# Kernel tuning notes

Hardware: AMD Instinct MI355X
Metric: run time of the kernel (lower is better)

## Reference

```python
import math
import jax, jax.numpy as jnp
import numpy as np

B, T, HID = 2, 1024, 2048
NH = 2            # num_householder
H = 6             # num_heads
DK = 256          # head_qk_dim
DV = 512          # head_v_dim (expand_v=2)
KEY_DIM = H * DK  # 1536
VAL_DIM = H * DV  # 3072
KCONV = 4
CHUNK = 64        # remat chunk for the scan


def _short_conv(x, w):
    # causal depthwise conv1d + silu. x: [B,T,C], w: [C,K]
    K = w.shape[-1]
    Tt = x.shape[1]
    xp = jnp.pad(x, ((0, 0), (K - 1, 0), (0, 0)))
    y = sum(xp[:, j:j + Tt, :] * w[:, j] for j in range(K))
    return jax.nn.silu(y)


def _interleave(seqs):
    b, t = seqs[0].shape[:2]
    return jnp.stack(seqs, axis=2).reshape(b, t * len(seqs), *seqs[0].shape[2:])


def _l2norm(x):
    return x * jax.lax.rsqrt(jnp.sum(x * x, axis=-1, keepdims=True) + 1e-12)


def _gated_delta_rule(q, k, v, g, beta):
    # q,k: [B,Ti,H,DK], v: [B,Ti,H,DV], g,beta: [B,Ti,H]
    tm = lambda x: jnp.moveaxis(x, 1, 0)  # time-major
    q, k, v, g, beta = map(tm, (q, k, v, g, beta))
    Ti, bsz = q.shape[0], q.shape[1]
    nc = Ti // CHUNK
    rc = lambda x: x.reshape(nc, CHUNK, *x.shape[1:])
    inputs = tuple(map(rc, (q, k, v, g, beta)))

    def step(S, inp):
        qt, kt, vt, gt, bt = inp
        S = S * jnp.exp(gt)[..., None, None]                      # forget gate
        err = vt - jnp.einsum('bhk,bhkv->bhv', kt, S)             # delta-rule error
        u = err * bt[..., None]
        S = S + jnp.einsum('bhk,bhv->bhkv', kt, u)                # rank-1 update
        o_t = jnp.einsum('bhk,bhkv->bhv', qt, S)
        return S, o_t

    @jax.checkpoint
    def chunk_fn(S, ci):
        return jax.lax.scan(step, S, ci)

    S0 = jnp.zeros((bsz, H, DK, DV), q.dtype)
    _, o = jax.lax.scan(chunk_fn, S0, inputs)
    o = o.reshape(Ti, bsz, H, DV)
    return jnp.moveaxis(o, 0, 1)


def setup_inputs() -> dict:
    key = jax.random.key(0)
    ks = jax.random.split(key, 16)
    s = 0.02
    dt = jnp.exp(jax.random.uniform(ks[12], (H,)) * (math.log(0.1) - math.log(0.001)) + math.log(0.001))
    dt = jnp.clip(dt, 1e-4, None)
    return {
        'hidden_states': jax.random.normal(ks[0], (B, T, HID), jnp.float32),
        'q_w': jax.random.normal(ks[1], (HID, KEY_DIM)) * s,
        'k_ws': jax.random.normal(ks[2], (NH, HID, KEY_DIM)) * s,
        'v_ws': jax.random.normal(ks[3], (NH, HID, VAL_DIM)) * s,
        'b_ws': jax.random.normal(ks[4], (NH, HID, H)) * s,
        'a_w': jax.random.normal(ks[5], (HID, H)) * s,
        'g_w': jax.random.normal(ks[6], (HID, VAL_DIM)) * s,
        'o_w': jax.random.normal(ks[7], (VAL_DIM, HID)) * s,
        'q_conv_w': jax.random.normal(ks[8], (KEY_DIM, KCONV)) * 0.3,
        'k_conv_ws': jax.random.normal(ks[9], (NH, KEY_DIM, KCONV)) * 0.3,
        'v_conv_ws': jax.random.normal(ks[10], (NH, VAL_DIM, KCONV)) * 0.3,
        'A_log': jnp.log(jax.random.uniform(ks[11], (H,), minval=0.5, maxval=16.0)),
        'dt_bias': dt + jnp.log(-jnp.expm1(-dt)),
        'o_norm_w': jnp.ones((DV,), jnp.float32),
    }


def reference(hidden_states, q_w, k_ws, v_ws, b_ws, a_w, g_w, o_w,
              q_conv_w, k_conv_ws, v_conv_ws, A_log, dt_bias, o_norm_w):
    x = hidden_states
    ks_list = [_short_conv(x @ k_ws[i], k_conv_ws[i]) for i in range(NH)]
    vs_list = [_short_conv(x @ v_ws[i], v_conv_ws[i]) for i in range(NH)]
    betas = [jax.nn.sigmoid(x @ b_ws[i]) for i in range(NH)]
    q = _short_conv(x @ q_w, q_conv_w)

    # interleave: q only at the last sub-step, g only at the first
    q_i = _interleave([jnp.zeros_like(q)] * (NH - 1) + [q])
    k_i = _interleave(ks_list)
    v_i = _interleave(vs_list)
    beta_i = _interleave(betas)
    g = -jnp.exp(A_log) * jax.nn.softplus(x @ a_w + dt_bias)   # [B,T,H]
    g_i = _interleave([g] + [jnp.zeros_like(g)] * (NH - 1))

    heads = lambda t, d: t.reshape(t.shape[0], t.shape[1], H, d)
    qh = _l2norm(heads(q_i, DK)) * (DK ** -0.5)
    kh = _l2norm(heads(k_i, DK))
    vh = heads(v_i, DV)

    o = _gated_delta_rule(qh, kh, vh, g_i, beta_i)   # [B,T*NH,H,DV]
    o = o[:, NH - 1::NH]                             # [B,T,H,DV]

    gate = heads(x @ g_w, DV)
    rms = o * jax.lax.rsqrt(jnp.mean(o * o, axis=-1, keepdims=True) + 1e-5) * o_norm_w
    o = rms * (gate * jax.nn.sigmoid(gate))          # RMSNorm + swish gate
    return o.reshape(B, T, VAL_DIM) @ o_w
```

## Files before the change

kernel.cpp:

```cpp
#include <hip/hip_runtime.h>


typedef short bf16x8 __attribute__((ext_vector_type(8)));
typedef short bf16x4 __attribute__((ext_vector_type(4)));
typedef float f32x4 __attribute__((ext_vector_type(4)));

__device__ __forceinline__ float bf2f(short s) {
  unsigned u = ((unsigned)(unsigned short)s) << 16;
  float f; __builtin_memcpy(&f, &u, 4); return f;
}
__device__ __forceinline__ short f2bf(float f) {
  unsigned u; __builtin_memcpy(&u, &f, 4);
  u = (u + 0x7FFFu + ((u >> 16) & 1u)) >> 16;
  return (short)u;
}
__device__ __forceinline__ f32x4 MFMA(bf16x8 a, bf16x8 b, f32x4 c) {
  return __builtin_amdgcn_mfma_f32_16x16x32_bf16(a, b, c, 0, 0, 0);
}
__device__ __forceinline__ void gl_lds16(const short* g, short* l) {
  __builtin_amdgcn_global_load_lds(
      (const __attribute__((address_space(1))) unsigned int*)g,
      (__attribute__((address_space(3))) unsigned int*)l, 16, 0, 0);
}

#define PJ_N 13824
#define NTOK 2048

__global__ __launch_bounds__(256) void cvt_bf16(
    const float* __restrict__ src, short* __restrict__ dst, int n)
{
  int i = (blockIdx.x * 256 + threadIdx.x) * 8;
  if (i + 8 <= n) {
    float4 a = *(const float4*)(src + i);
    float4 b = *(const float4*)(src + i + 4);
    short v[8] = {f2bf(a.x), f2bf(a.y), f2bf(a.z), f2bf(a.w),
                  f2bf(b.x), f2bf(b.y), f2bf(b.z), f2bf(b.w)};
    uint4 u; __builtin_memcpy(&u, v, 16);
    *(uint4*)(dst + i) = u;
  }
}

__global__ __launch_bounds__(256) void transpose_w(
    const float* __restrict__ W, short* __restrict__ WT, int K, int N)
{
  __shared__ short tile[64][68];
  const int n0 = blockIdx.x * 64, k0 = blockIdx.y * 64;
  const int lane = threadIdx.x & 63, wv = threadIdx.x >> 6;
  #pragma unroll
  for (int j = 0; j < 16; ++j) {
    int kk = wv * 16 + j;
    tile[kk][lane] = f2bf(W[(size_t)(k0 + kk) * N + n0 + lane]);
  }
  __syncthreads();
  const int nr = threadIdx.x >> 2, seg = (threadIdx.x & 3) * 16;
  short v[16];
  #pragma unroll
  for (int j = 0; j < 16; ++j) v[j] = tile[seg + j][nr];
  uint4 a, b; __builtin_memcpy(&a, v, 16); __builtin_memcpy(&b, v + 8, 16);
  short* dst = WT + (size_t)(n0 + nr) * K + k0 + seg;
  *(uint4*)dst = a;
  *(uint4*)(dst + 8) = b;
}

template<bool F32OUT>
__global__ __launch_bounds__(256) void gemm_bt(
    const short* __restrict__ A, const short* __restrict__ BT,
    void* __restrict__ Cp, int M, int N, int K)
{
  __shared__ short As[128 * 64];
  __shared__ short Bs[128 * 64];
  const int tid = threadIdx.x;
  const int lane = tid & 63, wv = tid >> 6;
  const int quad = lane >> 4, l16 = lane & 15;
  const int j = blockIdx.x;
  const int xcd = j & 7, local = j >> 3;
  const int mtile = local & 15, ng = local >> 4;
  const int ntile = ng * 8 + xcd;
  if (ntile * 128 >= N) return;
  const int m0 = mtile * 128, n0 = ntile * 128;
  const int wm = (wv >> 1) * 64, wn = (wv & 1) * 64;
  const int lrow = lane >> 3;
  const int lperm = (lane & 7) ^ lrow;
  const int xr = l16 & 7;
  f32x4 zz = {0.f, 0.f, 0.f, 0.f};
  f32x4 acc[4][4];
  #pragma unroll
  for (int i = 0; i < 4; ++i)
    #pragma unroll
    for (int jj = 0; jj < 4; ++jj) acc[i][jj] = zz;

  for (int k0 = 0; k0 < K; k0 += 64) {
    __syncthreads();
    #pragma unroll
    for (int c = 0; c < 4; ++c) {
      int row = (wv * 4 + c) * 8 + lrow;
      gl_lds16(A  + (size_t)(m0 + row) * K + k0 + lperm * 8,
               As + (wv * 4 + c) * 512);
      gl_lds16(BT + (size_t)(n0 + row) * K + k0 + lperm * 8,
               Bs + (wv * 4 + c) * 512);
    }
    __syncthreads();
    #pragma unroll
    for (int kk = 0; kk < 64; kk += 32) {
      const int ksb = kk >> 3;
      bf16x8 af[4], bfr[4];
      #pragma unroll
      for (int i = 0; i < 4; ++i)
        af[i] = *(const bf16x8*)(As + (wm + i * 16 + l16) * 64 +
                                 (((ksb + quad) ^ xr) << 3));
      #pragma unroll
      for (int jj = 0; jj < 4; ++jj)
        bfr[jj] = *(const bf16x8*)(Bs + (wn + jj * 16 + l16) * 64 +
                                   (((ksb + quad) ^ xr) << 3));
      #pragma unroll
      for (int i = 0; i < 4; ++i)
        #pragma unroll
        for (int jj = 0; jj < 4; ++jj)
          acc[i][jj] = MFMA(af[i], bfr[jj], acc[i][jj]);
    }
  }
  #pragma unroll
  for (int i = 0; i < 4; ++i)
    #pragma unroll
    for (int jj = 0; jj < 4; ++jj)
      #pragma unroll
      for (int r = 0; r < 4; ++r) {
        int row = m0 + wm + i * 16 + quad * 4 + r;
        int col = n0 + wn + jj * 16 + l16;
        if (F32OUT) ((float*)Cp)[(size_t)row * N + col] = acc[i][jj][r];
        else        ((short*)Cp)[(size_t)row * N + col] = f2bf(acc[i][jj][r]);
      }
}

__global__ __launch_bounds__(64) void proj_small(
    const float* __restrict__ x, const float* __restrict__ b_ws,
    const float* __restrict__ a_w, const float* __restrict__ A_log,
    const float* __restrict__ dt_bias,
    float* __restrict__ Beta0, float* __restrict__ Beta1, float* __restrict__ G)
{
  int row = blockIdx.x, lane = threadIdx.x;
  float p[18];
  #pragma unroll
  for (int j = 0; j < 18; ++j) p[j] = 0.f;
  for (int k = lane; k < 2048; k += 64) {
    float xv = x[(size_t)row * 2048 + k];
    const float* b0 = b_ws + (size_t)k * 6;
    const float* b1 = b_ws + (size_t)2048 * 6 + (size_t)k * 6;
    const float* aw = a_w + (size_t)k * 6;
    #pragma unroll
    for (int j = 0; j < 6; ++j) {
      p[j]      += xv * b0[j];
      p[6 + j]  += xv * b1[j];
      p[12 + j] += xv * aw[j];
    }
  }
  #pragma unroll
  for (int j = 0; j < 18; ++j) {
    #pragma unroll
    for (int off = 32; off > 0; off >>= 1)
      p[j] += __shfl_down(p[j], off);
  }
  if (lane == 0) {
    #pragma unroll
    for (int j = 0; j < 6; ++j) {
      Beta0[(size_t)row * 6 + j] = 1.f / (1.f + expf(-p[j]));
      Beta1[(size_t)row * 6 + j] = 1.f / (1.f + expf(-p[6 + j]));
      float z = p[12 + j] + dt_bias[j];
      float sp = (z > 15.f) ? z : log1pf(expf(z));
      G[(size_t)row * 6 + j] = -expf(A_log[j]) * sp;
    }
  }
}

__global__ __launch_bounds__(256) void conv_norm_qk(
    const short* __restrict__ P, const float* __restrict__ convw,
    short* __restrict__ dst, int colofs, float scale)
{
  __shared__ float red[256];
  int c = threadIdx.x, h = blockIdx.y, row = blockIdx.x;
  int t = row & 1023;
  int ch = colofs + h * 256 + c;
  const float* cw = convw + (size_t)(h * 256 + c) * 4;
  float acc = 0.f;
  #pragma unroll
  for (int j = 0; j < 4; ++j) {
    int tt = t - 3 + j;
    if (tt >= 0) acc += bf2f(P[(size_t)(row - 3 + j) * PJ_N + ch]) * cw[j];
  }
  float y = acc / (1.f + expf(-acc));
  red[c] = y * y;
  __syncthreads();
  for (int s = 128; s > 0; s >>= 1) {
    if (c < s) red[c] += red[c + s];
    __syncthreads();
  }
  float nrm = rsqrtf(red[0] + 1e-12f) * scale;
  dst[((size_t)row * 6 + h) * 256 + c] = f2bf(y * nrm);
}

__global__ __launch_bounds__(256) void conv_v(
    const short* __restrict__ P, const float* __restrict__ convw,
    short* __restrict__ dst, int colofs)
{
  int cg = blockIdx.y * 256 + threadIdx.x;
  int row = blockIdx.x;
  int t = row & 1023;
  const float* cw = convw + (size_t)cg * 4;
  float acc = 0.f;
  #pragma unroll
  for (int j = 0; j < 4; ++j) {
    int tt = t - 3 + j;
    if (tt >= 0) acc += bf2f(P[(size_t)(row - 3 + j) * PJ_N + colofs + cg]) * cw[j];
  }
  float y = acc / (1.f + expf(-acc));
  dst[(size_t)row * 3072 + cg] = f2bf(y);
}

#define KBLD 264
#define R2LD 72
#define WTLD 72
__global__ __launch_bounds__(256) void precompute_chunk(
    const short* __restrict__ Qc, const short* __restrict__ K0c, const short* __restrict__ K1c,
    const short* __restrict__ V0c, const short* __restrict__ V1c,
    const float* __restrict__ Beta0, const float* __restrict__ Beta1, const float* __restrict__ G,
    short* __restrict__ NTW, short* __restrict__ Qg, short* __restrict__ KdT,
    short* __restrict__ Mm, short* __restrict__ TBV, float* __restrict__ dC)
{
  __shared__ short r0[256 * 72];
  __shared__ float Xs[64 * 64];
  __shared__ short r2[64 * 72];
  const int tid = threadIdx.x;
  const int lane = tid & 63, wv = tid >> 6;
  const int quad = lane >> 4, l16 = lane & 15;
  const int c = blockIdx.x, h = blockIdx.y, b = blockIdx.z;
  const int i0 = c * 32;
  const size_t idx = (size_t)((b * 6 + h) * 32 + c);
  short* kb = r0;
  f32x4 zz = {0.f, 0.f, 0.f, 0.f};
  bf16x8 z8 = {0, 0, 0, 0, 0, 0, 0, 0};

  float gv, betaL;
  {
    int t = lane, par = t & 1, i = i0 + (t >> 1);
    size_t gofs = (size_t)(b * 1024 + i) * 6 + h;
    gv = par ? 0.f : G[gofs];
    betaL = par ? Beta1[gofs] : Beta0[gofs];
  }
  float cum = gv;
  #pragma unroll
  for (int off = 1; off < 64; off <<= 1) {
    float nb = __shfl_up(cum, off);
    if (lane >= off) cum += nb;
  }
  float c63 = __shfl(cum, 63);
  float eBt = expf(cum);
  float eRem = expf(c63 - cum);
  float wsc = betaL * eBt;
  if (tid == 0) dC[idx] = expf(c63);

  {
    int row = tid >> 2, seg = (tid & 3) * 64;
    int par = row & 1, i = i0 + (row >> 1);
    const short* src = (par ? K1c : K0c) + ((size_t)(b * 1024 + i) * 6 + h) * 256 + seg;
    short* dp = kb + row * KBLD + seg;
    #pragma unroll
    for (int e = 0; e < 64; e += 8)
      *(uint4*)(dp + e) = *(const uint4*)(src + e);
  }
  __syncthreads();

  {
    f32x4 acc[4];
    #pragma unroll
    for (int ts = 0; ts < 4; ++ts) acc[ts] = zz;
    #pragma unroll
    for (int ks = 0; ks < 8; ++ks) {
      bf16x8 af = *(const bf16x8*)(kb + (wv * 16 + l16) * KBLD + ks * 32 + quad * 8);
      #pragma unroll
      for (int ts = 0; ts < 4; ++ts) {
        bf16x8 bfv = *(const bf16x8*)(kb + (ts * 16 + l16) * KBLD + ks * 32 + quad * 8);
        acc[ts] = MFMA(af, bfv, acc[ts]);
      }
    }
    #pragma unroll
    for (int ts = 0; ts < 4; ++ts)
      #pragma unroll
      for (int r = 0; r < 4; ++r)
        r2[(wv * 16 + quad * 4 + r) * R2LD + ts * 16 + l16] = f2bf(acc[ts][r]);
  }
  {
    f32x4 acc[4];
    #pragma unroll
    for (int ts = 0; ts < 4; ++ts) acc[ts] = zz;
    int t_row = wv * 16 + l16;
    int podd = t_row & 1, iq = i0 + (t_row >> 1);
    const short* qrow = Qc + ((size_t)(b * 1024 + iq) * 6 + h) * 256;
    #pragma unroll
    for (int ks = 0; ks < 8; ++ks) {
      bf16x8 af = z8;
      if (podd) af = *(const bf16x8*)(qrow + ks * 32 + quad * 8);
      #pragma unroll
      for (int ts = 0; ts < 4; ++ts) {
        bf16x8 bfv = *(const bf16x8*)(kb + (ts * 16 + l16) * KBLD + ks * 32 + quad * 8);
        acc[ts] = MFMA(af, bfv, acc[ts]);
      }
    }
    short* Mp = Mm + idx * 2048;
    #pragma unroll
    for (int ts = 0; ts < 4; ++ts)
      #pragma unroll
      for (int r = 1; r < 4; r += 2) {
        int t = wv * 16 + quad * 4 + r, s = ts * 16 + l16;
        float ct = __shfl(cum, t), cs = __shfl(cum, s);
        float v = (s <= t) ? acc[ts][r] * expf(ct - cs) : 0.f;
        Mp[(t >> 1) * 64 + s] = f2bf(v);
      }
  }
  {
    int th = tid >> 3, dseg = (tid & 7) * 32;
    int t = th * 2 + 1;
    float sc = __shfl(eBt, t);
    const short* qrow = Qc + ((size_t)(b * 1024 + i0 + th) * 6 + h) * 256 + dseg;
    short* qgp = Qg + idx * 8192 + (size_t)th * 256 + dseg;
    #pragma unroll
    for (int e = 0; e < 32; e += 8) {
      bf16x8 v = *(const bf16x8*)(qrow + e);
      bf16x8 w;
      #pragma unroll
      for (int q2 = 0; q2 < 8; ++q2) w[q2] = f2bf(bf2f(v[q2]) * sc);
      *(bf16x8*)(qgp + e) = w;
    }
  }
  {
    int d = tid;
    short buf[64];
    #pragma unroll
    for (int t = 0; t < 64; ++t) {
      float sc = __shfl(eRem, t);
      buf[t] = f2bf(bf2f(kb[t * KBLD + d]) * sc);
    }
    short* kp = KdT + idx * 16384 + (size_t)d * 64;
    #pragma unroll
    for (int e = 0; e < 64; e += 8) {
      uint4 v; __builtin_memcpy(&v, buf + e, 16);
      *(uint4*)(kp + e) = v;
    }
  }
  __syncthreads();

  short colv[64];
  {
    int d = tid;
    #pragma unroll
    for (int t = 0; t < 64; ++t) colv[t] = kb[t * KBLD + d];
  }
  #pragma unroll
  for (int k = 0; k < 16; ++k) {
    int t = wv + k * 4;
    float bt = __shfl(betaL, t);
    float ct = __shfl(cum, t);
    float a = (lane < t) ? bt * expf(ct - cum) * bf2f(r2[t * R2LD + lane]) : 0.f;
    Xs[t * 64 + lane] = a;
  }
  __syncthreads();
  {
    int d = tid;
    short wrow[64];
    #pragma unroll
    for (int s = 0; s < 64; ++s) wrow[s] = f2bf(bf2f(colv[s]) * __shfl(wsc, s));
    short* wp = r0 + d * WTLD;
    #pragma unroll
    for (int e = 0; e < 64; e += 8) {
      uint4 v; __builtin_memcpy(&v, wrow + e, 16);
      *(uint4*)(wp + e) = v;
    }
  }
  if (wv == 0) {
    const int j = lane;
    float xcol[64];
    #pragma unroll
    for (int t = 0; t < 64; ++t) {
      float sa0 = 0.f, sa1 = 0.f;
      const float2* ap = (const float2*)(Xs + t * 64);
      #pragma unroll
      for (int s = 0; s + 1 < t; s += 2) {
        float2 av = ap[s >> 1];
        sa0 += av.x * xcol[s];
        sa1 += av.y * xcol[s + 1];
      }
      if (t & 1) sa0 += Xs[t * 64 + (t - 1)] * xcol[t - 1];
      float xv = ((t == j) ? 1.f : 0.f) - (sa0 + sa1);
      xcol[t] = xv;
      r2[t * R2LD + j] = f2bf(xv);
    }
  }
  __syncthreads();
  {
    f32x4 acc[4][4];
    #pragma unroll
    for (int i = 0; i < 4; ++i)
      #pragma unroll
      for (int j = 0; j < 4; ++j) acc[i][j] = zz;
    #pragma unroll
    for (int ks = 0; ks < 2; ++ks) {
      bf16x8 af[4], bfv[4];
      #pragma unroll
      for (int tt = 0; tt < 4; ++tt)
        af[tt] = *(const bf16x8*)(r2 + (tt * 16 + l16) * R2LD + ks * 32 + quad * 8);
      #pragma unroll
      for (int dt = 0; dt < 4; ++dt)
        bfv[dt] = *(const bf16x8*)(r0 + ((wv * 4 + dt) * 16 + l16) * WTLD + ks * 32 + quad * 8);
      #pragma unroll
      for (int tt = 0; tt < 4; ++tt)
        #pragma unroll
        for (int dt = 0; dt < 4; ++dt)
          acc[tt][dt] = MFMA(af[tt], bfv[dt], acc[tt][dt]);
    }
    short* np = NTW + idx * 16384;
    #pragma unroll
    for (int tt = 0; tt < 4; ++tt)
      #pragma unroll
      for (int dt = 0; dt < 4; ++dt)
        #pragma unroll
        for (int r = 0; r < 4; ++r) {
          int t = tt * 16 + quad * 4 + r, d = (wv * 4 + dt) * 16 + l16;
          np[t * 256 + d] = f2bf(-acc[tt][dt][r]);
        }
  }
  __syncthreads();
  for (int vh = 0; vh < 2; ++vh) {
    {
      int vl = tid;
      short bv[64];
      #pragma unroll
      for (int t = 0; t < 64; ++t) {
        int par = t & 1, i = i0 + (t >> 1);
        const short* src = (par ? V1c : V0c) + (size_t)(b * 1024 + i) * 3072 + h * 512 + vh * 256 + vl;
        bv[t] = f2bf(bf2f(*src) * __shfl(betaL, t));
      }
      short* bp = r0 + vl * WTLD;
      #pragma unroll
      for (int e = 0; e < 64; e += 8) {
        uint4 v; __builtin_memcpy(&v, bv + e, 16);
        *(uint4*)(bp + e) = v;
      }
    }
    __syncthreads();
    {
      f32x4 acc[4][4];
      #pragma unroll
      for (int i = 0; i < 4; ++i)
        #pragma unroll
        for (int j = 0; j < 4; ++j) acc[i][j] = zz;
      #pragma unroll
      for (int ks = 0; ks < 2; ++ks) {
        bf16x8 af[4], bfv[4];
        #pragma unroll
        for (int tt = 0; tt < 4; ++tt)
          af[tt] = *(const bf16x8*)(r2 + (tt * 16 + l16) * R2LD + ks * 32 + quad * 8);
        #pragma unroll
        for (int vt = 0; vt < 4; ++vt)
          bfv[vt] = *(const bf16x8*)(r0 + ((wv * 4 + vt) * 16 + l16) * WTLD + ks * 32 + quad * 8);
        #pragma unroll
        for (int tt = 0; tt < 4; ++tt)
          #pragma unroll
          for (int vt = 0; vt < 4; ++vt)
            acc[tt][vt] = MFMA(af[tt], bfv[vt], acc[tt][vt]);
      }
      short* tp = TBV + idx * 32768;
      #pragma unroll
      for (int tt = 0; tt < 4; ++tt)
        #pragma unroll
        for (int vt = 0; vt < 4; ++vt) {
          int vfull = vh * 256 + (wv * 4 + vt) * 16 + l16;
          int t0 = tt * 16 + quad * 4;
          short w[4];
          #pragma unroll
          for (int r = 0; r < 4; ++r) w[r] = f2bf(acc[tt][vt][r]);
          uint2 uv; __builtin_memcpy(&uv, w, 8);
          *(uint2*)(tp + (size_t)vfull * 64 + t0) = uv;
        }
    }
    __syncthreads();
  }
}

#define SLD 264
#define ULD 72
__global__ __launch_bounds__(128) void scan_kernel(
    const short* __restrict__ NTW, const short* __restrict__ Qg,
    const short* __restrict__ KdT, const short* __restrict__ Mm,
    const short* __restrict__ TBV, const float* __restrict__ dC,
    short* __restrict__ O)
{
  __shared__ short NTWs[2][64 * 256];
  __shared__ short S[16 * SLD];
  __shared__ short U[16 * ULD];
  const int tid = threadIdx.x;
  const int lane = tid & 63, w = tid >> 6;
  const int quad = lane >> 4, l16 = lane & 15;
  const int xk = l16 & 7;
  const int r2l = lane >> 5;
  const int s32 = lane & 31;
  const int gid = (blockIdx.x & 7) * 48 + (blockIdx.x >> 3);
  const int bh = gid >> 5, slice = gid & 31;
  const int b = bh / 6, h = bh % 6;
  const int vbase = slice * 16;
  f32x4 zz = {0.f, 0.f, 0.f, 0.f};
  for (int e = tid; e < 16 * SLD; e += 128) S[e] = 0;

  {
    const short* ntw0 = NTW + (size_t)(bh * 32) * 16384;
    #pragma unroll
    for (int j = 0; j < 16; ++j) {
      int row = 32 * w + 2 * j + r2l;
      gl_lds16(ntw0 + (size_t)row * 256 + ((s32 ^ (row & 7)) << 3),
               &NTWs[0][(32 * w + 2 * j) * 256]);
    }
  }
  __syncthreads();

  for (int c = 0; c < 32; ++c) {
    size_t idx = (size_t)(bh * 32 + c);
    const short* qg  = Qg  + idx * 8192;
    const short* kdt = KdT + idx * 16384;
    const short* mp  = Mm  + idx * 2048;
    const short* tb  = TBV + idx * 32768;
    short* bufC = &NTWs[c & 1][0];
    short* bufN = &NTWs[(c & 1) ^ 1][0];
    const int cn = (c + 1) & 31;
    const short* ntwN = NTW + (size_t)(bh * 32 + cn) * 16384;

    asm volatile("s_waitcnt vmcnt(4)" ::: "memory");
    __builtin_amdgcn_sched_barrier(0);

    float dc = dC[idx];
    bf16x8 qgr[8];
    #pragma unroll
    for (int ks = 0; ks < 8; ++ks)
      qgr[ks] = *(const bf16x8*)(
          qg + (size_t)(w * 16 + l16) * 256 + ks * 32 + quad * 8);
    bf16x8 mmr2[2];
    #pragma unroll
    for (int ks = 0; ks < 2; ++ks)
      mmr2[ks] = *(const bf16x8*)(mp + (w * 16 + l16) * 64 + ks * 32 + quad * 8);
    bf16x4 tbv2[2];
    #pragma unroll
    for (int j = 0; j < 2; ++j)
      tbv2[j] = *(const bf16x4*)(
          tb + (size_t)(vbase + l16) * 64 + (2 * w + j) * 16 + quad * 4);
    bf16x8 kdr2[2][2][4];
    #pragma unroll
    for (int j = 0; j < 2; ++j)
      #pragma unroll
      for (int ks = 0; ks < 2; ++ks)
        #pragma unroll
        for (int dt = 0; dt < 4; ++dt)
          kdr2[j][ks][dt] = *(const bf16x8*)(
              kdt + (size_t)(((2 * w + j) * 4 + dt) * 16 + l16) * 64 + ks * 32 + quad * 8);
    __builtin_amdgcn_sched_barrier(0);

    #pragma unroll
    for (int j = 0; j < 16; ++j) {
      int row = 32 * w + 2 * j + r2l;
      gl_lds16(ntwN + (size_t)row * 256 + ((s32 ^ (row & 7)) << 3),
               bufN + (32 * w + 2 * j) * 256);
    }
    __builtin_amdgcn_sched_barrier(0);

    f32x4 uA0 = zz, uB0 = zz, uA1 = zz, uB1 = zz;
    __builtin_amdgcn_s_setprio(1);
    #pragma unroll
    for (int ks = 0; ks < 4; ++ks) {
      bf16x8 bfv0 = *(const bf16x8*)(S + l16 * SLD + ks * 32 + quad * 8);
      bf16x8 bfv1 = *(const bf16x8*)(S + l16 * SLD + (ks + 4) * 32 + quad * 8);
      int gx0 = ks * 4 + quad, gx1 = (ks + 4) * 4 + quad;
      bf16x8 a00 = *(const bf16x8*)(bufC + ((2 * w + 0) * 16 + l16) * 256 + ((gx0 ^ xk) << 3));
      bf16x8 a01 = *(const bf16x8*)(bufC + ((2 * w + 0) * 16 + l16) * 256 + ((gx1 ^ xk) << 3));
      bf16x8 a10 = *(const bf16x8*)(bufC + ((2 * w + 1) * 16 + l16) * 256 + ((gx0 ^ xk) << 3));
      bf16x8 a11 = *(const bf16x8*)(bufC + ((2 * w + 1) * 16 + l16) * 256 + ((gx1 ^ xk) << 3));
      uA0 = MFMA(a00, bfv0, uA0);
      uB0 = MFMA(a01, bfv1, uB0);
      uA1 = MFMA(a10, bfv0, uA1);
      uB1 = MFMA(a11, bfv1, uB1);
    }
    __builtin_amdgcn_s_setprio(0);
    f32x4 uac2[2];
    #pragma unroll
    for (int r = 0; r < 4; ++r) { uac2[0][r] = uA0[r] + uB0[r]; uac2[1][r] = uA1[r] + uB1[r]; }

    asm volatile("s_waitcnt vmcnt(32)" ::: "memory");
    __builtin_amdgcn_sched_barrier(0);

    #pragma unroll
    for (int j = 0; j < 2; ++j) {
      short wb[4];
      #pragma unroll
      for (int r = 0; r < 4; ++r) wb[r] = f2bf(uac2[j][r] + bf2f(tbv2[j][r]));
      uint2 uv; __builtin_memcpy(&uv, wb, 8);
      *(uint2*)(U + l16 * ULD + (2 * w + j) * 16 + quad * 4) = uv;
    }
    asm volatile("s_waitcnt lgkmcnt(0)" ::: "memory");
    __builtin_amdgcn_s_barrier();
    __builtin_amdgcn_sched_barrier(0);

    f32x4 oA = zz, oB = zz;
    #pragma unroll
    for (int ks = 0; ks < 4; ++ks) {
      bf16x8 bfv0 = *(const bf16x8*)(S + l16 * SLD + ks * 32 + quad * 8);
      bf16x8 bfv1 = *(const bf16x8*)(S + l16 * SLD + (ks + 4) * 32 + quad * 8);
      oA = MFMA(qgr[ks], bfv0, oA);
      oB = MFMA(qgr[ks + 4], bfv1, oB);
    }
    {
      bf16x8 ub0 = *(const bf16x8*)(U + l16 * ULD + 0 * 32 + quad * 8);
      bf16x8 ub1 = *(const bf16x8*)(U + l16 * ULD + 1 * 32 + quad * 8);
      oA = MFMA(mmr2[0], ub0, oA);
      oB = MFMA(mmr2[1], ub1, oB);
    }
    f32x4 oac;
    #pragma unroll
    for (int r = 0; r < 4; ++r) oac[r] = oA[r] + oB[r];

    #pragma unroll
    for (int r = 0; r < 4; ++r) {
      int th = w * 16 + quad * 4 + r;
      int i = c * 32 + th;
      O[((size_t)(b * 1024 + i) * 6 + h) * 512 + vbase + l16] = f2bf(oac[r]);
    }

    asm volatile("s_waitcnt vmcnt(20)" ::: "memory");
    __builtin_amdgcn_sched_barrier(0);

    asm volatile("s_waitcnt lgkmcnt(0)" ::: "memory");
    __builtin_amdgcn_s_barrier();
    __builtin_amdgcn_sched_barrier(0);

    __builtin_amdgcn_s_setprio(1);
    #pragma unroll
    for (int j = 0; j < 2; ++j) {
      const int g2 = 2 * w + j;
      f32x4 sac[4];
      #pragma unroll
      for (int dt = 0; dt < 4; ++dt) {
        bf16x4 sv = *(const bf16x4*)(S + l16 * SLD + (g2 * 4 + dt) * 16 + quad * 4);
        #pragma unroll
        for (int r = 0; r < 4; ++r) sac[dt][r] = dc * bf2f(sv[r]);
      }
      #pragma unroll
      for (int ks = 0; ks < 2; ++ks) {
        bf16x8 bfv = *(const bf16x8*)(U + l16 * ULD + ks * 32 + quad * 8);
        #pragma unroll
        for (int dt = 0; dt < 4; ++dt)
          sac[dt] = MFMA(kdr2[j][ks][dt], bfv, sac[dt]);
      }
      #pragma unroll
      for (int dt = 0; dt < 4; ++dt) {
        short wb[4];
        #pragma unroll
        for (int r = 0; r < 4; ++r) wb[r] = f2bf(sac[dt][r]);
        uint2 uv; __builtin_memcpy(&uv, wb, 8);
        *(uint2*)(S + l16 * SLD + (g2 * 4 + dt) * 16 + quad * 4) = uv;
      }
    }
    __builtin_amdgcn_s_setprio(0);
    asm volatile("s_waitcnt lgkmcnt(0)" ::: "memory");
    __builtin_amdgcn_s_barrier();
    __builtin_amdgcn_sched_barrier(0);
  }
}

__global__ __launch_bounds__(256) void rms_gate(
    const short* __restrict__ O, const short* __restrict__ P,
    const float* __restrict__ onw, short* __restrict__ OutPre)
{
  __shared__ float red[256];
  int tid = threadIdx.x, h = blockIdx.y, row = blockIdx.x;
  size_t base = ((size_t)row * 6 + h) * 512;
  float a = bf2f(O[base + tid]), b2 = bf2f(O[base + 256 + tid]);
  red[tid] = a * a + b2 * b2;
  __syncthreads();
  for (int s = 128; s > 0; s >>= 1) {
    if (tid < s) red[tid] += red[tid + s];
    __syncthreads();
  }
  float r = rsqrtf(red[0] * (1.f / 512.f) + 1e-5f);
  #pragma unroll
  for (int half = 0; half < 2; ++half) {
    int col = tid + half * 256;
    float ov = half ? b2 : a;
    float g = bf2f(P[(size_t)row * PJ_N + 10752 + h * 512 + col]);
    float sg = g / (1.f + expf(-g));
    OutPre[(size_t)row * 3072 + h * 512 + col] = f2bf(ov * r * onw[col] * sg);
  }
}

extern "C" void kernel_launch(void* const* d_in, const int* in_sizes, int n_in,
                              void* d_out, int out_size, void* d_ws, size_t ws_size,
                              hipStream_t stream) {
  const float* x        = (const float*)d_in[0];
  const float* q_w      = (const float*)d_in[1];
  const float* k_ws     = (const float*)d_in[2];
  const float* v_ws     = (const float*)d_in[3];
  const float* b_ws     = (const float*)d_in[4];
  const float* a_w      = (const float*)d_in[5];
  const float* g_w      = (const float*)d_in[6];
  const float* o_w      = (const float*)d_in[7];
  const float* q_conv_w = (const float*)d_in[8];
  const float* k_conv   = (const float*)d_in[9];
  const float* v_conv   = (const float*)d_in[10];
  const float* A_log    = (const float*)d_in[11];
  const float* dt_bias  = (const float*)d_in[12];
  const float* o_norm_w = (const float*)d_in[13];
  float* out = (float*)d_out;

  char* ws = (char*)d_ws;
  size_t off = 0;
  auto take = [&](size_t bytes) {
    size_t r = off;
    off += (bytes + 255) & ~(size_t)255;
    return r;
  };
  short* P  = (short*)(ws + take((size_t)NTOK * PJ_N * 2));
  short* oT = (short*)(ws + take((size_t)2048 * 3072 * 2));
  size_t regX = take((size_t)NTOK * 2048 * 2);
  short* xbf = (short*)(ws + regX);
  short* Mm  = (short*)(ws + regX);
  size_t regA = take((size_t)PJ_N * 2048 * 2);
  short* WTall = (short*)(ws + regA);
  short* NTW = (short*)(ws + regA);
  short* Qg  = NTW + (size_t)384 * 16384;
  short* KdT = Qg  + (size_t)384 * 8192;
  short* TBV = KdT + (size_t)384 * 16384;
  size_t regB = take((size_t)44040192);
  short* Qc  = (short*)(ws + regB);
  short* K0c = Qc  + (size_t)NTOK * 1536;
  short* K1c = K0c + (size_t)NTOK * 1536;
  short* V0c = K1c + (size_t)NTOK * 1536;
  short* V1c = V0c + (size_t)NTOK * 3072;
  short* O      = (short*)(ws + regB);
  short* OutPre = O + (size_t)NTOK * 6 * 512;
  float* Beta0 = (float*)(ws + take((size_t)NTOK * 6 * 4));
  float* Beta1 = (float*)(ws + take((size_t)NTOK * 6 * 4));
  float* G     = (float*)(ws + take((size_t)NTOK * 6 * 4));
  float* dCp   = (float*)(ws + take((size_t)384 * 4));
  if (off > ws_size) return;

  cvt_bf16<<<dim3(NTOK * 2048 / 8 / 256), 256, 0, stream>>>(x, xbf, NTOK * 2048);

  transpose_w<<<dim3(24, 32), 256, 0, stream>>>(q_w, WTall, 2048, 1536);
  transpose_w<<<dim3(24, 32), 256, 0, stream>>>(k_ws, WTall + (size_t)1536 * 2048, 2048, 1536);
  transpose_w<<<dim3(24, 32), 256, 0, stream>>>(k_ws + (size_t)2048 * 1536, WTall + (size_t)3072 * 2048, 2048, 1536);
  transpose_w<<<dim3(48, 32), 256, 0, stream>>>(v_ws, WTall + (size_t)4608 * 2048, 2048, 3072);
  transpose_w<<<dim3(48, 32), 256, 0, stream>>>(v_ws + (size_t)2048 * 3072, WTall + (size_t)7680 * 2048, 2048, 3072);
  transpose_w<<<dim3(48, 32), 256, 0, stream>>>(g_w, WTall + (size_t)10752 * 2048, 2048, 3072);
  transpose_w<<<dim3(32, 48), 256, 0, stream>>>(o_w, oT, 3072, 2048);

  gemm_bt<false><<<dim3(16 * 112), 256, 0, stream>>>(
      xbf, WTall, P, NTOK, PJ_N, 2048);

  proj_small<<<dim3(NTOK), 64, 0, stream>>>(x, b_ws, a_w, A_log, dt_bias, Beta0, Beta1, G);

  conv_norm_qk<<<dim3(NTOK, 6), 256, 0, stream>>>(P, q_conv_w, Qc, 0, 0.0625f);
  conv_norm_qk<<<dim3(NTOK, 6), 256, 0, stream>>>(P, k_conv, K0c, 1536, 1.f);
  conv_norm_qk<<<dim3(NTOK, 6), 256, 0, stream>>>(P, k_conv + (size_t)1536 * 4, K1c, 3072, 1.f);
  conv_v<<<dim3(NTOK, 12), 256, 0, stream>>>(P, v_conv, V0c, 4608);
  conv_v<<<dim3(NTOK, 12), 256, 0, stream>>>(P, v_conv + (size_t)3072 * 4, V1c, 7680);

  precompute_chunk<<<dim3(32, 6, 2), 256, 0, stream>>>(Qc, K0c, K1c, V0c, V1c,
      Beta0, Beta1, G, NTW, Qg, KdT, Mm, TBV, dCp);

  scan_kernel<<<dim3(384), 128, 0, stream>>>(NTW, Qg, KdT, Mm, TBV, dCp, O);

  rms_gate<<<dim3(NTOK, 6), 256, 0, stream>>>(O, P, o_norm_w, OutPre);

  gemm_bt<true><<<dim3(16 * 16), 256, 0, stream>>>(
      OutPre, oT, out, NTOK, 2048, 3072);
}
```

Baseline: 804.9 us.

## Store Qg, KdT and TBV in MFMA-fragment order so scan loads coalesce

```diff
diff --git a/kernel.cpp b/kernel.cpp
--- a/kernel.cpp
+++ b/kernel.cpp
@@ -144,14 +144,15 @@
   for (int j = 0; j < 18; ++j) p[j] = 0.f;
   for (int k = lane; k < 2048; k += 64) {
     float xv = x[(size_t)row * 2048 + k];
-    const float* b0 = b_ws + (size_t)k * 6;
-    const float* b1 = b_ws + (size_t)2048 * 6 + (size_t)k * 6;
-    const float* aw = a_w + (size_t)k * 6;
-    #pragma unroll
-    for (int j = 0; j < 6; ++j) {
-      p[j]      += xv * b0[j];
-      p[6 + j]  += xv * b1[j];
-      p[12 + j] += xv * aw[j];
+    const float2* b0 = (const float2*)(b_ws + (size_t)k * 6);
+    const float2* b1 = (const float2*)(b_ws + (size_t)2048 * 6 + (size_t)k * 6);
+    const float2* aw = (const float2*)(a_w + (size_t)k * 6);
+    #pragma unroll
+    for (int j = 0; j < 3; ++j) {
+      float2 v0 = b0[j], v1 = b1[j], v2 = aw[j];
+      p[2 * j]      += xv * v0.x; p[2 * j + 1]      += xv * v0.y;
+      p[6 + 2 * j]  += xv * v1.x; p[6 + 2 * j + 1]  += xv * v1.y;
+      p[12 + 2 * j] += xv * v2.x; p[12 + 2 * j + 1] += xv * v2.y;
     }
   }
   #pragma unroll
@@ -317,18 +318,19 @@
       }
   }
   {
-    int th = tid >> 3, dseg = (tid & 7) * 32;
+    int w2 = tid >> 7, ksq = (tid >> 4) & 7, l16q = tid & 15;
+    int th = w2 * 16 + l16q;
     int t = th * 2 + 1;
     float sc = __shfl(eBt, t);
-    const short* qrow = Qc + ((size_t)(b * 1024 + i0 + th) * 6 + h) * 256 + dseg;
-    short* qgp = Qg + idx * 8192 + (size_t)th * 256 + dseg;
-    #pragma unroll
-    for (int e = 0; e < 32; e += 8) {
-      bf16x8 v = *(const bf16x8*)(qrow + e);
-      bf16x8 w;
-      #pragma unroll
-      for (int q2 = 0; q2 < 8; ++q2) w[q2] = f2bf(bf2f(v[q2]) * sc);
-      *(bf16x8*)(qgp + e) = w;
+    const short* qrow = Qc + ((size_t)(b * 1024 + i0 + th) * 6 + h) * 256;
+    short* qgp = Qg + idx * 8192;
+    #pragma unroll
+    for (int qd = 0; qd < 4; ++qd) {
+      bf16x8 v = *(const bf16x8*)(qrow + ksq * 32 + qd * 8);
+      bf16x8 w8;
+      #pragma unroll
+      for (int q2 = 0; q2 < 8; ++q2) w8[q2] = f2bf(bf2f(v[q2]) * sc);
+      *(bf16x8*)(qgp + ((size_t)((w2 * 8 + ksq) * 64 + qd * 16 + l16q)) * 8) = w8;
     }
   }
   {
@@ -339,12 +341,15 @@
       float sc = __shfl(eRem, t);
       buf[t] = f2bf(bf2f(kb[t * KBLD + d]) * sc);
     }
-    short* kp = KdT + idx * 16384 + (size_t)d * 64;
-    #pragma unroll
-    for (int e = 0; e < 64; e += 8) {
-      uint4 v; __builtin_memcpy(&v, buf + e, 16);
-      *(uint4*)(kp + e) = v;
-    }
+    int dblk = d >> 4, l16k = d & 15;
+    short* kp = KdT + idx * 16384;
+    #pragma unroll
+    for (int ks = 0; ks < 2; ++ks)
+      #pragma unroll
+      for (int qd = 0; qd < 4; ++qd) {
+        uint4 v; __builtin_memcpy(&v, buf + ks * 32 + qd * 8, 16);
+        *(uint4*)(kp + ((size_t)((dblk * 2 + ks) * 64 + qd * 16 + l16k)) * 8) = v;
+      }
   }
   __syncthreads();
 
@@ -472,13 +477,12 @@
       for (int tt = 0; tt < 4; ++tt)
         #pragma unroll
         for (int vt = 0; vt < 4; ++vt) {
-          int vfull = vh * 256 + (wv * 4 + vt) * 16 + l16;
-          int t0 = tt * 16 + quad * 4;
+          int S = vh * 16 + wv * 4 + vt;
           short w[4];
           #pragma unroll
           for (int r = 0; r < 4; ++r) w[r] = f2bf(acc[tt][vt][r]);
           uint2 uv; __builtin_memcpy(&uv, w, 8);
-          *(uint2*)(tp + (size_t)vfull * 64 + t0) = uv;
+          *(uint2*)(tp + ((size_t)((S * 4 + tt) * 64 + quad * 16 + l16)) * 4) = uv;
         }
     }
     __syncthreads();
@@ -538,8 +542,7 @@
     bf16x8 qgr[8];
     #pragma unroll
     for (int ks = 0; ks < 8; ++ks)
-      qgr[ks] = *(const bf16x8*)(
-          qg + (size_t)(w * 16 + l16) * 256 + ks * 32 + quad * 8);
+      qgr[ks] = *(const bf16x8*)(qg + ((size_t)((w * 8 + ks) * 64 + lane)) * 8);
     bf16x8 mmr2[2];
     #pragma unroll
     for (int ks = 0; ks < 2; ++ks)
@@ -547,8 +550,7 @@
     bf16x4 tbv2[2];
     #pragma unroll
     for (int j = 0; j < 2; ++j)
-      tbv2[j] = *(const bf16x4*)(
-          tb + (size_t)(vbase + l16) * 64 + (2 * w + j) * 16 + quad * 4);
+      tbv2[j] = *(const bf16x4*)(tb + ((size_t)((slice * 4 + 2 * w + j) * 64 + lane)) * 4);
     bf16x8 kdr2[2][2][4];
     #pragma unroll
     for (int j = 0; j < 2; ++j)
@@ -557,7 +559,7 @@
         #pragma unroll
         for (int dt = 0; dt < 4; ++dt)
           kdr2[j][ks][dt] = *(const bf16x8*)(
-              kdt + (size_t)(((2 * w + j) * 4 + dt) * 16 + l16) * 64 + ks * 32 + quad * 8);
+              kdt + ((size_t)((((2 * w + j) * 4 + dt) * 2 + ks) * 64 + lane)) * 8);
     __builtin_amdgcn_sched_barrier(0);
 
     #pragma unroll
```

Measured after the change: 740.0 us, median of 2. -8.1%, faster.
